# Performance work log

Hardware: AMD Instinct MI355X
Metric: run time of the kernel (lower is better)

## Reference

```python
import jax, jax.numpy as jnp
import numpy as np

B, S, E, H, D = 2, 4096, 512, 8, 64  # batch, seq, embed, heads, key_dim


def setup_inputs() -> dict:
    key = jax.random.key(0)
    ks = jax.random.split(key, 8)
    queries = jax.random.normal(ks[0], (B, S, E), dtype=jnp.float32)
    keys = jax.random.normal(ks[1], (B, S, E), dtype=jnp.float32)
    values = jax.random.normal(ks[2], (B, S, E), dtype=jnp.float32)
    mask = jax.random.randint(ks[3], (B, H, S, S), 0, 2).astype(bool)
    scale = 1.0 / np.sqrt(E)
    Wq = jax.random.normal(ks[4], (E, H * D), dtype=jnp.float32) * scale
    Wk = jax.random.normal(ks[5], (E, H * D), dtype=jnp.float32) * scale
    Wv = jax.random.normal(ks[6], (E, H * D), dtype=jnp.float32) * scale
    Wo = jax.random.normal(ks[7], (H * D, E), dtype=jnp.float32) * scale
    return {"queries": queries, "keys": keys, "values": values, "mask": mask,
            "Wq": Wq, "Wk": Wk, "Wv": Wv, "Wo": Wo}


def reference(queries, keys, values, mask, Wq, Wk, Wv, Wo):
    # QKV projections (no bias), reshape to heads: (B, S, H, D)
    q = (queries @ Wq).reshape(B, -1, H, D)
    k = (keys @ Wk).reshape(B, -1, H, D)
    v = (values @ Wv).reshape(B, -1, H, D)
    # scores: (B, H, Sq, Sk)
    scores = jnp.einsum("bqhd,bkhd->bhqk", q, k) / jnp.sqrt(jnp.float32(D))
    scores = jnp.where(mask, jnp.float32(-1e10), scores)
    attn = jax.nn.softmax(scores, axis=-1)
    out = jnp.einsum("bhqk,bkhd->bqhd", attn, v).reshape(B, -1, H * D)
    return out @ Wo
```

## Files before the change

kernel.cpp:

```cpp
#include <hip/hip_runtime.h>
#include <hip/hip_bf16.h>

#define NB 2
#define NS 4096
#define NE 512
#define NH 8
#define ND 64
#define NHD 512

typedef __attribute__((ext_vector_type(8))) short short8;
typedef __attribute__((ext_vector_type(4))) float floatx4;

#define MFMA16(a, b, c) __builtin_amdgcn_mfma_f32_16x16x32_bf16((a), (b), (c), 0, 0, 0)

union Cvt8 { uint4 u; short8 s; };
static __device__ __forceinline__ short8 ld8(const __hip_bfloat16* p) {
  Cvt8 c; c.u = *(const uint4*)p; return c.s;
}
union BH { __hip_bfloat16 h; short s; };
static __device__ __forceinline__ short f2bs(float x) {
  BH u; u.h = __float2bfloat16(x); return u.s;
}

__global__ __launch_bounds__(256) void wconv(
    const float* w0, const float* w1, const float* w2, const float* w3,
    __hip_bfloat16* t0, __hip_bfloat16* t1,
    __hip_bfloat16* t2, __hip_bfloat16* t3) {
  __shared__ __hip_bfloat16 tile[64][72];
  const float* src;
  __hip_bfloat16* dst;
  switch (blockIdx.z) {
    case 0: src = w0; dst = t0; break;
    case 1: src = w1; dst = t1; break;
    case 2: src = w2; dst = t2; break;
    default: src = w3; dst = t3; break;
  }
  const int tx = threadIdx.x & 63, ty = threadIdx.x >> 6;
  const int n0 = blockIdx.x * 64, k0 = blockIdx.y * 64;
  for (int r = ty; r < 64; r += 4)
    tile[r][tx] = __float2bfloat16(src[(long)(k0 + r) * 512 + n0 + tx]);
  __syncthreads();
  for (int r = ty; r < 64; r += 4)
    dst[(long)(n0 + r) * 512 + k0 + tx] = tile[tx][r];
}

__global__ __launch_bounds__(256) void gemm_qkv(
    const float* A0, const float* A1, const float* A2,
    const __hip_bfloat16* W0, const __hip_bfloat16* W1, const __hip_bfloat16* W2,
    __hip_bfloat16* O0, __hip_bfloat16* O1, __hip_bfloat16* O2) {
  const float* A;
  const __hip_bfloat16* Wt;
  __hip_bfloat16* O;
  switch (blockIdx.z) {
    case 0: A = A0; Wt = W0; O = O0; break;
    case 1: A = A1; Wt = W1; O = O1; break;
    default: A = A2; Wt = W2; O = O2; break;
  }
  const int lane = threadIdx.x & 63;
  const int w = threadIdx.x >> 6;
  const int c = lane & 15, g = lane >> 4;
  const int m0 = blockIdx.x * 64 + w * 16;
  const int n0 = blockIdx.y * 64;

  floatx4 acc[4] = {};
  const float* ap = A + (long)(m0 + c) * 512 + g * 8;
  const __hip_bfloat16* wp = Wt + (long)(n0 + c) * 512 + g * 8;
  for (int ks = 0; ks < 512; ks += 32) {
    const float4 f0 = *(const float4*)(ap + ks);
    const float4 f1 = *(const float4*)(ap + ks + 4);
    short8 a;
    a[0] = f2bs(f0.x); a[1] = f2bs(f0.y); a[2] = f2bs(f0.z); a[3] = f2bs(f0.w);
    a[4] = f2bs(f1.x); a[5] = f2bs(f1.y); a[6] = f2bs(f1.z); a[7] = f2bs(f1.w);
#pragma unroll
    for (int t = 0; t < 4; ++t) {
      short8 b = ld8(wp + t * 16 * 512 + ks);
      acc[t] = MFMA16(a, b, acc[t]);
    }
  }
#pragma unroll
  for (int t = 0; t < 4; ++t) {
#pragma unroll
    for (int r = 0; r < 4; ++r) {
      const int m = m0 + g * 4 + r;
      const int n = n0 + t * 16 + c;
      const int bb = m >> 12, s = m & 4095, h = n >> 6, d = n & 63;
      O[(((long)bb * NH + h) * NS + s) * ND + d] = __float2bfloat16(acc[t][r]);
    }
  }
}

#define VPAD 72
__device__ __forceinline__ int vswz(int row) { return ((row >> 3) & 7) * 8; }

__global__ __launch_bounds__(256) void flash_attn(
    const __hip_bfloat16* Q, const __hip_bfloat16* K, const __hip_bfloat16* V,
    const int* mask, __hip_bfloat16* AO) {
  __shared__ __hip_bfloat16 Ks[64 * VPAD];
  __shared__ __hip_bfloat16 Vt[64 * VPAD];
  __shared__ __hip_bfloat16 Pb[4 * 16 * VPAD];

  const int tid = threadIdx.x;
  const int lane = tid & 63, w = tid >> 6;
  const int c = lane & 15, g = lane >> 4;
  const int bz = blockIdx.z, hy = blockIdx.y;
  const int q0 = blockIdx.x * 64 + w * 16;
  const long headbase = ((long)bz * NH + hy) * NS;

  const short8 qf0 = ld8(Q + (headbase + q0 + c) * ND + g * 8);
  const short8 qf1 = ld8(Q + (headbase + q0 + c) * ND + 32 + g * 8);

  floatx4 oacc[4] = {};
  float m_i[4], l_i[4];
#pragma unroll
  for (int r = 0; r < 4; ++r) { m_i[r] = -1e30f; l_i[r] = 0.f; }
  __hip_bfloat16* Pw = Pb + w * 16 * VPAD;

  for (int kt = 0; kt < 64; ++kt) {
    const int k0 = kt * 64;
#pragma unroll
    for (int it = 0; it < 2; ++it) {
      const int chunk = tid + it * 256;
      const int kc = chunk >> 3;
      const int dd = (chunk & 7) * 8;
      const long gbase = (headbase + k0 + kc) * ND + dd;
      *(uint4*)&Ks[kc * VPAD + dd] = *(const uint4*)(K + gbase);
      uint4 vv = *(const uint4*)(V + gbase);
      const __hip_bfloat16* ve = (const __hip_bfloat16*)&vv;
#pragma unroll
      for (int j = 0; j < 8; ++j) {
        const int row = dd + j;
        Vt[row * VPAD + (kc ^ vswz(row))] = ve[j];
      }
    }
    __syncthreads();

    floatx4 sacc[4] = {};
#pragma unroll
    for (int t = 0; t < 4; ++t) {
      short8 b0 = ld8(&Ks[(t * 16 + c) * VPAD + g * 8]);
      sacc[t] = MFMA16(qf0, b0, sacc[t]);
      short8 b1 = ld8(&Ks[(t * 16 + c) * VPAD + 32 + g * 8]);
      sacc[t] = MFMA16(qf1, b1, sacc[t]);
    }

    float alpha[4];
#pragma unroll
    for (int r = 0; r < 4; ++r) {
      const int qrow = q0 + g * 4 + r;
      const int* mrow = mask + (headbase + qrow) * NS + k0 + c;
      float mx = -1e30f;
#pragma unroll
      for (int t = 0; t < 4; ++t) {
        float s = sacc[t][r] * 0.125f;
        if (mrow[t * 16] != 0) s = -1e10f;
        sacc[t][r] = s;
        mx = fmaxf(mx, s);
      }
#pragma unroll
      for (int off = 1; off < 16; off <<= 1)
        mx = fmaxf(mx, __shfl_xor(mx, off));
      const float mn = fmaxf(m_i[r], mx);
      const float al = __expf(m_i[r] - mn);
      float ps = 0.f;
#pragma unroll
      for (int t = 0; t < 4; ++t) {
        const float p = __expf(sacc[t][r] - mn);
        sacc[t][r] = p;
        ps += p;
      }
#pragma unroll
      for (int off = 1; off < 16; off <<= 1)
        ps += __shfl_xor(ps, off);
      m_i[r] = mn;
      l_i[r] = l_i[r] * al + ps;
      alpha[r] = al;
#pragma unroll
      for (int t = 0; t < 4; ++t)
        Pw[(g * 4 + r) * VPAD + t * 16 + c] = __float2bfloat16(sacc[t][r]);
    }

#pragma unroll
    for (int t = 0; t < 4; ++t)
#pragma unroll
      for (int r = 0; r < 4; ++r) oacc[t][r] *= alpha[r];

    __syncthreads();

#pragma unroll
    for (int ks2 = 0; ks2 < 2; ++ks2) {
      short8 af = ld8(&Pw[c * VPAD + ks2 * 32 + g * 8]);
#pragma unroll
      for (int t = 0; t < 4; ++t) {
        const int row = t * 16 + c;
        short8 bf = ld8(&Vt[row * VPAD + ((ks2 * 32 + g * 8) ^ vswz(row))]);
        oacc[t] = MFMA16(af, bf, oacc[t]);
      }
    }
    __syncthreads();
  }

#pragma unroll
  for (int t = 0; t < 4; ++t) {
#pragma unroll
    for (int r = 0; r < 4; ++r) {
      const int qrow = q0 + g * 4 + r;
      const float v = oacc[t][r] / l_i[r];
      AO[((long)bz * NS + qrow) * NHD + hy * 64 + t * 16 + c] = __float2bfloat16(v);
    }
  }
}

__global__ __launch_bounds__(256) void gemm_out(
    const __hip_bfloat16* A, const __hip_bfloat16* Wt, float* O) {
  const int lane = threadIdx.x & 63;
  const int w = threadIdx.x >> 6;
  const int c = lane & 15, g = lane >> 4;
  const int m0 = blockIdx.x * 64 + w * 16;
  const int n0 = blockIdx.y * 64;

  floatx4 acc[4] = {};
  const __hip_bfloat16* ap = A + (long)(m0 + c) * 512 + g * 8;
  const __hip_bfloat16* wp = Wt + (long)(n0 + c) * 512 + g * 8;
  for (int ks = 0; ks < 512; ks += 32) {
    short8 a = ld8(ap + ks);
#pragma unroll
    for (int t = 0; t < 4; ++t) {
      short8 b = ld8(wp + t * 16 * 512 + ks);
      acc[t] = MFMA16(a, b, acc[t]);
    }
  }
#pragma unroll
  for (int t = 0; t < 4; ++t)
#pragma unroll
    for (int r = 0; r < 4; ++r)
      O[(long)(m0 + g * 4 + r) * 512 + n0 + t * 16 + c] = acc[t][r];
}

extern "C" void kernel_launch(void* const* d_in, const int* in_sizes, int n_in,
                              void* d_out, int out_size, void* d_ws, size_t ws_size,
                              hipStream_t stream) {
  const float* q_in = (const float*)d_in[0];
  const float* k_in = (const float*)d_in[1];
  const float* v_in = (const float*)d_in[2];
  const int* mask = (const int*)d_in[3];
  const float* Wq = (const float*)d_in[4];
  const float* Wk = (const float*)d_in[5];
  const float* Wv = (const float*)d_in[6];
  const float* Wo = (const float*)d_in[7];
  float* out = (float*)d_out;

  char* base = (char*)d_ws;
  const size_t MB = 1u << 20;
  __hip_bfloat16* wtq = (__hip_bfloat16*)(base);
  __hip_bfloat16* wtk = (__hip_bfloat16*)(base + 512 * 1024);
  __hip_bfloat16* wtv = (__hip_bfloat16*)(base + 1 * MB);
  __hip_bfloat16* wto = (__hip_bfloat16*)(base + 1 * MB + 512 * 1024);
  __hip_bfloat16* qp = (__hip_bfloat16*)(base + 2 * MB);
  __hip_bfloat16* kp = (__hip_bfloat16*)(base + 10 * MB);
  __hip_bfloat16* vp = (__hip_bfloat16*)(base + 18 * MB);
  __hip_bfloat16* ao = (__hip_bfloat16*)(base + 26 * MB);

  wconv<<<dim3(8, 8, 4), 256, 0, stream>>>(Wq, Wk, Wv, Wo, wtq, wtk, wtv, wto);
  gemm_qkv<<<dim3(128, 8, 3), 256, 0, stream>>>(
      q_in, k_in, v_in, wtq, wtk, wtv, qp, kp, vp);
  flash_attn<<<dim3(NS / 64, NH, NB), 256, 0, stream>>>(qp, kp, vp, mask, ao);
  gemm_out<<<dim3(128, 8), 256, 0, stream>>>(ao, wto, out);
}
```

Measured before the change: 1.619 ms.

## Pack attention mask into bitmasks and skip rescale when row max is unchanged

Adds a pre-pass kernel that uses wavefront ballots to compress the int32 mask into 64-bit words, one word per 64 keys of a query row. The attention kernel then reads one word per row per key tile instead of scattered int loads. The 1/sqrt(D) scale is folded into the Q projection epilogue. The online softmax now skips the alpha rescale when no row max grows, and a __syncthreads before the PV step is dropped. The cost is an extra kernel that still streams the full int mask, in exchange for much less mask traffic and work inside the attention loop.

```diff
diff --git a/kernel.cpp b/kernel.cpp
--- a/kernel.cpp
+++ b/kernel.cpp
@@ -20,6 +20,28 @@
 union BH { __hip_bfloat16 h; short s; };
 static __device__ __forceinline__ short f2bs(float x) {
   BH u; u.h = __float2bfloat16(x); return u.s;
+}
+
+__global__ __launch_bounds__(256) void mask_pack(const int* __restrict__ mask,
+                                                 unsigned long long* __restrict__ bits) {
+  const int lane = threadIdx.x & 63;
+  const long wid = (long)((blockIdx.x * 256 + threadIdx.x) >> 6);
+  const long base = wid * 512;
+  const int* p = mask + base * 64 + lane;
+  for (int i = 0; i < 512; i += 4) {
+    const int m0 = p[(long)(i + 0) * 64];
+    const int m1 = p[(long)(i + 1) * 64];
+    const int m2 = p[(long)(i + 2) * 64];
+    const int m3 = p[(long)(i + 3) * 64];
+    const unsigned long long b0 = __ballot(m0 != 0);
+    const unsigned long long b1 = __ballot(m1 != 0);
+    const unsigned long long b2 = __ballot(m2 != 0);
+    const unsigned long long b3 = __ballot(m3 != 0);
+    if (lane == 0) {
+      *(ulonglong2*)(bits + base + i) = ulonglong2{b0, b1};
+      *(ulonglong2*)(bits + base + i + 2) = ulonglong2{b2, b3};
+    }
+  }
 }
 
 __global__ __launch_bounds__(256) void wconv(
@@ -77,6 +99,7 @@
       acc[t] = MFMA16(a, b, acc[t]);
     }
   }
+  const float sc = (blockIdx.z == 0) ? 0.125f : 1.0f;
 #pragma unroll
   for (int t = 0; t < 4; ++t) {
 #pragma unroll
@@ -84,7 +107,7 @@
       const int m = m0 + g * 4 + r;
       const int n = n0 + t * 16 + c;
       const int bb = m >> 12, s = m & 4095, h = n >> 6, d = n & 63;
-      O[(((long)bb * NH + h) * NS + s) * ND + d] = __float2bfloat16(acc[t][r]);
+      O[(((long)bb * NH + h) * NS + s) * ND + d] = __float2bfloat16(acc[t][r] * sc);
     }
   }
 }
@@ -94,7 +117,7 @@
 
 __global__ __launch_bounds__(256) void flash_attn(
     const __hip_bfloat16* Q, const __hip_bfloat16* K, const __hip_bfloat16* V,
-    const int* mask, __hip_bfloat16* AO) {
+    const unsigned long long* __restrict__ Mb, __hip_bfloat16* AO) {
   __shared__ __hip_bfloat16 Ks[64 * VPAD];
   __shared__ __hip_bfloat16 Vt[64 * VPAD];
   __shared__ __hip_bfloat16 Pb[4 * 16 * VPAD];
@@ -105,6 +128,7 @@
   const int bz = blockIdx.z, hy = blockIdx.y;
   const int q0 = blockIdx.x * 64 + w * 16;
   const long headbase = ((long)bz * NH + hy) * NS;
+  const unsigned long long* mrp0 = Mb + ((headbase + q0 + g * 4) << 6);
 
   const short8 qf0 = ld8(Q + (headbase + q0 + c) * ND + g * 8);
   const short8 qf1 = ld8(Q + (headbase + q0 + c) * ND + 32 + g * 8);
@@ -134,6 +158,12 @@
     }
     __syncthreads();
 
+    unsigned long long mrow[4];
+    mrow[0] = mrp0[kt];
+    mrow[1] = mrp0[64 + kt];
+    mrow[2] = mrp0[128 + kt];
+    mrow[3] = mrp0[192 + kt];
+
     floatx4 sacc[4] = {};
 #pragma unroll
     for (int t = 0; t < 4; ++t) {
@@ -143,48 +173,70 @@
       sacc[t] = MFMA16(qf1, b1, sacc[t]);
     }
 
-    float alpha[4];
+    float mx[4];
 #pragma unroll
     for (int r = 0; r < 4; ++r) {
-      const int qrow = q0 + g * 4 + r;
-      const int* mrow = mask + (headbase + qrow) * NS + k0 + c;
-      float mx = -1e30f;
-#pragma unroll
-      for (int t = 0; t < 4; ++t) {
-        float s = sacc[t][r] * 0.125f;
-        if (mrow[t * 16] != 0) s = -1e10f;
-        sacc[t][r] = s;
-        mx = fmaxf(mx, s);
+      const unsigned long long ms = mrow[r] >> c;
+      float s0 = ((unsigned)ms & 1u) ? -1e10f : sacc[0][r];
+      float s1 = ((unsigned)(ms >> 16) & 1u) ? -1e10f : sacc[1][r];
+      float s2 = ((unsigned)(ms >> 32) & 1u) ? -1e10f : sacc[2][r];
+      float s3 = ((unsigned)(ms >> 48) & 1u) ? -1e10f : sacc[3][r];
+      sacc[0][r] = s0; sacc[1][r] = s1; sacc[2][r] = s2; sacc[3][r] = s3;
+      float mxr = fmaxf(fmaxf(s0, s1), fmaxf(s2, s3));
+#pragma unroll
+      for (int off = 1; off < 16; off <<= 1)
+        mxr = fmaxf(mxr, __shfl_xor(mxr, off));
+      mx[r] = mxr;
+    }
+
+    const bool grow = (mx[0] > m_i[0]) | (mx[1] > m_i[1]) |
+                      (mx[2] > m_i[2]) | (mx[3] > m_i[3]);
+    if (__ballot(grow) != 0ull) {
+      float alpha[4];
+#pragma unroll
+      for (int r = 0; r < 4; ++r) {
+        const float mn = fmaxf(m_i[r], mx[r]);
+        const float al = __expf(m_i[r] - mn);
+        float ps = 0.f;
+#pragma unroll
+        for (int t = 0; t < 4; ++t) {
+          const float p = __expf(sacc[t][r] - mn);
+          sacc[t][r] = p;
+          ps += p;
+        }
+#pragma unroll
+        for (int off = 1; off < 16; off <<= 1)
+          ps += __shfl_xor(ps, off);
+        m_i[r] = mn;
+        l_i[r] = l_i[r] * al + ps;
+        alpha[r] = al;
       }
 #pragma unroll
-      for (int off = 1; off < 16; off <<= 1)
-        mx = fmaxf(mx, __shfl_xor(mx, off));
-      const float mn = fmaxf(m_i[r], mx);
-      const float al = __expf(m_i[r] - mn);
-      float ps = 0.f;
-#pragma unroll
-      for (int t = 0; t < 4; ++t) {
-        const float p = __expf(sacc[t][r] - mn);
-        sacc[t][r] = p;
-        ps += p;
+      for (int t = 0; t < 4; ++t)
+#pragma unroll
+        for (int r = 0; r < 4; ++r) oacc[t][r] *= alpha[r];
+    } else {
+#pragma unroll
+      for (int r = 0; r < 4; ++r) {
+        float ps = 0.f;
+#pragma unroll
+        for (int t = 0; t < 4; ++t) {
+          const float p = __expf(sacc[t][r] - m_i[r]);
+          sacc[t][r] = p;
+          ps += p;
+        }
+#pragma unroll
+        for (int off = 1; off < 16; off <<= 1)
+          ps += __shfl_xor(ps, off);
+        l_i[r] += ps;
       }
-#pragma unroll
-      for (int off = 1; off < 16; off <<= 1)
-        ps += __shfl_xor(ps, off);
-      m_i[r] = mn;
-      l_i[r] = l_i[r] * al + ps;
-      alpha[r] = al;
+    }
+
+#pragma unroll
+    for (int r = 0; r < 4; ++r)
 #pragma unroll
       for (int t = 0; t < 4; ++t)
         Pw[(g * 4 + r) * VPAD + t * 16 + c] = __float2bfloat16(sacc[t][r]);
-    }
-
-#pragma unroll
-    for (int t = 0; t < 4; ++t)
-#pragma unroll
-      for (int r = 0; r < 4; ++r) oacc[t][r] *= alpha[r];
-
-    __syncthreads();
 
 #pragma unroll
     for (int ks2 = 0; ks2 < 2; ++ks2) {
@@ -259,10 +311,12 @@
   __hip_bfloat16* kp = (__hip_bfloat16*)(base + 10 * MB);
   __hip_bfloat16* vp = (__hip_bfloat16*)(base + 18 * MB);
   __hip_bfloat16* ao = (__hip_bfloat16*)(base + 26 * MB);
-
+  unsigned long long* mb = (unsigned long long*)(base + 34 * MB);
+
+  mask_pack<<<dim3(2048), 256, 0, stream>>>(mask, mb);
   wconv<<<dim3(8, 8, 4), 256, 0, stream>>>(Wq, Wk, Wv, Wo, wtq, wtk, wtv, wto);
   gemm_qkv<<<dim3(128, 8, 3), 256, 0, stream>>>(
       q_in, k_in, v_in, wtq, wtk, wtv, qp, kp, vp);
-  flash_attn<<<dim3(NS / 64, NH, NB), 256, 0, stream>>>(qp, kp, vp, mask, ao);
+  flash_attn<<<dim3(NS / 64, NH, NB), 256, 0, stream>>>(qp, kp, vp, mb, ao);
   gemm_out<<<dim3(128, 8), 256, 0, stream>>>(ao, wto, out);
 }
```

New measurement: 1.897 ms. +17.2%, slower.
